# Performance work log

Measured on AMD Instinct MI355X. Metric: run time of the kernel, lower is better.

## Reference

```python
import jax, jax.numpy as jnp
import numpy as np

N_USERS, N_ITEMS, N_TOPICS = 200000, 100000, 100
N_NODES = N_USERS + N_ITEMS + N_TOPICS
N_EDGES = 5000000
DIM = 64
LAYERS = 3
BATCH = 16384


def setup_inputs() -> dict:
    key = jax.random.key(0)
    ks = jax.random.split(key, 8)
    users = jax.random.randint(ks[0], (BATCH,), 0, N_USERS, dtype=jnp.int64 if jax.config.jax_enable_x64 else jnp.int32)
    items = jax.random.randint(ks[1], (BATCH,), 0, N_ITEMS, dtype=jnp.int64 if jax.config.jax_enable_x64 else jnp.int32)
    edge_rows = jax.random.randint(ks[2], (N_EDGES,), 0, N_NODES, dtype=jnp.int32)
    edge_cols = jax.random.randint(ks[3], (N_EDGES,), 0, N_NODES, dtype=jnp.int32)
    # values ~ 1/deg to mimic the symmetric-normalized A_hat of LightGCN
    edge_vals = jax.random.uniform(ks[4], (N_EDGES,), dtype=jnp.float32) / 16.0
    user_emb = 0.1 * jax.random.normal(ks[5], (N_USERS, DIM), dtype=jnp.float32)
    item_emb = 0.1 * jax.random.normal(ks[6], (N_ITEMS, DIM), dtype=jnp.float32)
    topic_emb = 0.1 * jax.random.normal(ks[7], (N_TOPICS, DIM), dtype=jnp.float32)
    return {"users": users, "items": items, "edge_rows": edge_rows,
            "edge_cols": edge_cols, "edge_vals": edge_vals,
            "user_emb": user_emb, "item_emb": item_emb, "topic_emb": topic_emb}


def reference(users, items, edge_rows, edge_cols, edge_vals, user_emb, item_emb, topic_emb):
    n_users = user_emb.shape[0]
    n_nodes = n_users + item_emb.shape[0] + topic_emb.shape[0]
    # E^0 = [users; items; topics]
    h = jnp.concatenate([user_emb, item_emb, topic_emb], axis=0)  # [N, dim]
    acc = h
    for _ in range(LAYERS):
        # sparse A_hat @ h : gather source rows, scale by edge weight, scatter-add to dst
        msgs = edge_vals[:, None] * h[edge_cols]                  # [E, dim]
        h = jax.ops.segment_sum(msgs, edge_rows, num_segments=n_nodes)
        acc = acc + h
    out = acc / (LAYERS + 1)                                      # stack-mean over layers
    u = out[users]                                                # [B, dim]
    it = out[n_users + items]                                     # items offset into node table
    return jnp.sum(u * it, axis=1)                                # [B]
```

## Files before the change

kernel.cpp:

```cpp
#include <hip/hip_runtime.h>
#include <hip/hip_fp16.h>

#define N_USERS  200000
#define N_ITEMS  100000
#define N_TOPICS 100
#define N_NODES  (N_USERS + N_ITEMS + N_TOPICS)
#define DIM      64
#define BSHIFT   10
#define BROWS    (1 << BSHIFT)
#define NBUCKETS ((N_NODES + BROWS - 1) >> BSHIFT)
#define COLMASK  0x7FFFF
#define NB       512
#define NBSHIFT  9
#define M_TOT    (NBUCKETS * NB)
#define SB       256
#define CH       ((M_TOT + SB - 1) / SB)
#define BUCKET_CAP 24576



__global__ void prep_kernel(const int* __restrict__ rows,
                            int* __restrict__ partial, int n_edges,
                            const float* __restrict__ uemb,
                            const float* __restrict__ iemb,
                            const float* __restrict__ temb,
                            ushort* __restrict__ h0) {
    __shared__ int h[NBUCKETS];
    if (blockIdx.x < NB) {
        for (int i = threadIdx.x; i < NBUCKETS; i += blockDim.x) h[i] = 0;
        __syncthreads();
        int stride = NB * blockDim.x;
        for (int e = blockIdx.x * blockDim.x + threadIdx.x; e < n_edges; e += stride)
            atomicAdd(&h[((unsigned)rows[e]) >> BSHIFT], 1);
        __syncthreads();
        for (int i = threadIdx.x; i < NBUCKETS; i += blockDim.x)
            partial[blockIdx.x * NBUCKETS + i] = h[i];
    } else {
        int g = (blockIdx.x - NB) * blockDim.x + threadIdx.x;
        long base = (long)g * 4;
        if (base >= (long)N_NODES * DIM) return;
        const float* src;
        long off;
        if (base < (long)N_USERS * DIM)                 { src = uemb; off = base; }
        else if (base < (long)(N_USERS + N_ITEMS) * DIM){ src = iemb; off = base - (long)N_USERS * DIM; }
        else                                            { src = temb; off = base - (long)(N_USERS + N_ITEMS) * DIM; }
        float4 v = *(const float4*)(src + off);
        __half2 a = __floats2half2_rn(v.x, v.y);
        __half2 b = __floats2half2_rn(v.z, v.w);
        uint2 o;
        o.x = *(unsigned*)&a;
        o.y = *(unsigned*)&b;
        ((uint2*)h0)[g] = o;
    }
}

__device__ __forceinline__ int phys_idx(int L) {
    return (L & (NB - 1)) * NBUCKETS + (L >> NBSHIFT);
}

__global__ void scanB1_kernel(const int* __restrict__ partial,
                              int* __restrict__ psum) {
    __shared__ int s[256];
    int tid = threadIdx.x;
    int c0 = blockIdx.x * CH;
    int c1 = min(M_TOT, c0 + CH);
    int sum = 0;
    for (int L = c0 + tid; L < c1; L += 256) sum += partial[phys_idx(L)];
    s[tid] = sum;
    __syncthreads();
    for (int off = 128; off > 0; off >>= 1) {
        if (tid < off) s[tid] += s[tid + off];
        __syncthreads();
    }
    if (tid == 0) psum[blockIdx.x] = s[0];
}

__global__ void scanB3_kernel(const int* __restrict__ partial,
                              const int* __restrict__ psum,
                              int* __restrict__ offs) {
    __shared__ int s[SB];
    __shared__ int tile[256];
    __shared__ int carry;
    int tid = threadIdx.x;
    s[tid] = (tid < blockIdx.x) ? psum[tid] : 0;
    __syncthreads();
    for (int off = 128; off > 0; off >>= 1) {
        if (tid < off) s[tid] += s[tid + off];
        __syncthreads();
    }
    if (tid == 0) carry = s[0];
    __syncthreads();
    int c0 = blockIdx.x * CH;
    int c1 = min(M_TOT, c0 + CH);
    for (int base = c0; base < c1; base += 256) {
        int L = base + tid;
        int v = (L < c1) ? partial[phys_idx(L)] : 0;
        tile[tid] = v;
        __syncthreads();
        for (int off = 1; off < 256; off <<= 1) {
            int t = (tid >= off) ? tile[tid - off] : 0;
            __syncthreads();
            tile[tid] += t;
            __syncthreads();
        }
        if (L < c1) offs[L] = carry + tile[tid] - v;
        __syncthreads();
        if (tid == 255) carry += tile[255];
        __syncthreads();
    }
}

__global__ void scatter1_kernel(const int* __restrict__ rows,
                                const int* __restrict__ cols,
                                const float* __restrict__ vals,
                                const int* __restrict__ offs,
                                int2* __restrict__ bkt_buf, int n_edges) {
    __shared__ int lpos[NBUCKETS];
    for (int i = threadIdx.x; i < NBUCKETS; i += blockDim.x)
        lpos[i] = offs[i * NB + blockIdx.x];
    __syncthreads();
    int stride = gridDim.x * blockDim.x;
    for (int e = blockIdx.x * blockDim.x + threadIdx.x; e < n_edges; e += stride) {
        int r = rows[e];
        int b = ((unsigned)r) >> BSHIFT;
        int pos = atomicAdd(&lpos[b], 1);
        int2 p;
        p.x = cols[e] | ((r & (BROWS - 1)) << 19);
        p.y = __float_as_int(vals[e]);
        bkt_buf[pos] = p;
    }
}

__device__ __forceinline__ int pad8(int x) { return (x + 7) & ~7; }

__global__ void scatter2_kernel(const int2* __restrict__ bkt_buf,
                                const int* __restrict__ offs,
                                int2* __restrict__ row_span,
                                int2* __restrict__ csr_cv, int n_edges) {
    __shared__ int lcnt[BROWS];
    __shared__ int lptr[BROWS];
    __shared__ int lfill[BROWS];
    __shared__ int s[512];
    int b = blockIdx.x;
    int t = threadIdx.x;
    int e0 = offs[b * NB];
    int e1 = (b == NBUCKETS - 1) ? n_edges : offs[(b + 1) * NB];
    for (int i = t; i < BROWS; i += 512) { lcnt[i] = 0; lfill[i] = 0; }
    __syncthreads();
    for (int e = e0 + t; e < e1; e += blockDim.x)
        atomicAdd(&lcnt[((unsigned)bkt_buf[e].x) >> 19], 1);
    __syncthreads();
    s[t] = pad8(lcnt[2 * t]) + pad8(lcnt[2 * t + 1]);
    __syncthreads();
    for (int off = 1; off < 512; off <<= 1) {
        int v = (t >= off) ? s[t - off] : 0;
        __syncthreads();
        s[t] += v;
        __syncthreads();
    }
    {
        int base = b * BUCKET_CAP + (t ? s[t - 1] : 0);
        int rbase = b << BSHIFT;
        int pe = pad8(lcnt[2 * t]);
        int po = pad8(lcnt[2 * t + 1]);
        int p_even = base;
        int p_odd  = base + pe;
        lptr[2 * t]     = p_even;
        lptr[2 * t + 1] = p_odd;
        if (rbase + 2 * t < N_NODES) {
            int2 sp; sp.x = p_even; sp.y = p_even + pe;
            row_span[rbase + 2 * t] = sp;
        }
        if (rbase + 2 * t + 1 < N_NODES) {
            int2 sp; sp.x = p_odd; sp.y = p_odd + po;
            row_span[rbase + 2 * t + 1] = sp;
        }
    }
    __syncthreads();
    for (int e = e0 + t; e < e1; e += blockDim.x) {
        int2 p = bkt_buf[e];
        int delta = ((unsigned)p.x) >> 19;
        int pos = lptr[delta] + atomicAdd(&lfill[delta], 1);
        int2 cv;
        cv.x = p.x & COLMASK;
        cv.y = p.y;
        csr_cv[pos] = cv;
    }
    __syncthreads();
    for (int i = t; i < BROWS; i += 512) {
        int c  = lcnt[i];
        int cp = pad8(c);
        int p  = lptr[i];
        int2 z; z.x = 0; z.y = 0;
        for (int k = c; k < cp; ++k) csr_cv[p + k] = z;
    }
}

__device__ __forceinline__ float4 fma_mix4(const ushort* __restrict__ h,
                                           int row, int l16, float w,
                                           float4 acc) {
    uint2 r = ((const uint2*)(h + (size_t)row * DIM))[l16];
    __half2 h01 = *(__half2*)&r.x;
    __half2 h23 = *(__half2*)&r.y;
    acc.x = __builtin_fmaf(__half2float(__low2half(h01)),  w, acc.x);
    acc.y = __builtin_fmaf(__half2float(__high2half(h01)), w, acc.y);
    acc.z = __builtin_fmaf(__half2float(__low2half(h23)),  w, acc.z);
    acc.w = __builtin_fmaf(__half2float(__high2half(h23)), w, acc.w);
    return acc;
}

__device__ __forceinline__ float4 batch8(const int2* __restrict__ csr_cv,
                                         const ushort* __restrict__ h_src,
                                         int p, int l16, float4 acc) {
    const int4* q = (const int4*)(csr_cv + p);
    int4 a = q[0], b = q[1], c = q[2], d = q[3];
    acc = fma_mix4(h_src, a.x, l16, __int_as_float(a.y), acc);
    acc = fma_mix4(h_src, a.z, l16, __int_as_float(a.w), acc);
    acc = fma_mix4(h_src, b.x, l16, __int_as_float(b.y), acc);
    acc = fma_mix4(h_src, b.z, l16, __int_as_float(b.w), acc);
    acc = fma_mix4(h_src, c.x, l16, __int_as_float(c.y), acc);
    acc = fma_mix4(h_src, c.z, l16, __int_as_float(c.w), acc);
    acc = fma_mix4(h_src, d.x, l16, __int_as_float(d.y), acc);
    acc = fma_mix4(h_src, d.z, l16, __int_as_float(d.w), acc);
    return acc;
}

#define NWAVES ((N_NODES + 3) / 4)

__global__ void spmv_csr_kernel(const int2* __restrict__ row_span,
                                const int2* __restrict__ csr_cv,
                                const ushort* __restrict__ h_src,
                                ushort* __restrict__ h_dst,
                                const int* __restrict__ users,
                                const int* __restrict__ items,
                                float* __restrict__ u_acc,
                                float* __restrict__ it_acc,
                                int B, int first) {
    int wave = (int)(((long)blockIdx.x * blockDim.x + threadIdx.x) >> 6);
    int lane = threadIdx.x & 63;
    int g    = lane >> 4;
    int l16  = lane & 15;
    if (wave < NWAVES) {
        int r    = wave * 4 + g;
        int rc   = min(r, N_NODES - 1);
        int2 sp  = row_span[rc];
        int p0   = sp.x;
        int len  = (r < N_NODES) ? (sp.y - sp.x) : 0;
        int m = max(len, __shfl_xor(len, 16, 64));
        m = max(m, __shfl_xor(m, 32, 64));
        float4 acc = make_float4(0.f, 0.f, 0.f, 0.f);
        for (int off = 0; off < m; off += 8) {
            if (off < len)
                acc = batch8(csr_cv, h_src, p0 + off, l16, acc);
        }
        if (r < N_NODES) {
            __half2 a = __floats2half2_rn(acc.x, acc.y);
            __half2 b = __floats2half2_rn(acc.z, acc.w);
            uint2 o;
            o.x = *(unsigned*)&a;
            o.y = *(unsigned*)&b;
            ((uint2*)(h_dst + (size_t)r * DIM))[l16] = o;
        }
    } else {
        int s = (wave - NWAVES) * 4 + g;
        if (s >= 2 * B) return;
        int node = (s < B) ? users[s] : (N_USERS + items[s - B]);
        uint2 hr = ((const uint2*)(h_src + (size_t)node * DIM))[l16];
        float2 a01 = __half22float2(*(__half2*)&hr.x);
        float2 a23 = __half22float2(*(__half2*)&hr.y);
        float* dst = (s < B) ? (u_acc + (size_t)s * DIM)
                             : (it_acc + (size_t)(s - B) * DIM);
        float4* p = (float4*)dst + l16;
        if (first) {
            *p = make_float4(a01.x, a01.y, a23.x, a23.y);
        } else {
            float4 o = *p;
            o.x += a01.x; o.y += a01.y; o.z += a23.x; o.w += a23.y;
            *p = o;
        }
    }
}

__global__ void spmv_batch_kernel(const int2* __restrict__ row_span,
                                  const int2* __restrict__ csr_cv,
                                  const ushort* __restrict__ h_src,
                                  const int* __restrict__ users,
                                  const int* __restrict__ items,
                                  float* __restrict__ u_acc,
                                  float* __restrict__ it_acc, int B) {
    int wave = (int)(((long)blockIdx.x * blockDim.x + threadIdx.x) >> 6);
    int lane = threadIdx.x & 63;
    int g    = lane >> 4;
    int l16  = lane & 15;
    int s    = wave * 4 + g;
    bool ok  = s < 2 * B;
    int node = 0;
    if (ok) node = (s < B) ? users[s] : (N_USERS + items[s - B]);
    float4 acc = make_float4(0.f, 0.f, 0.f, 0.f);
    if (ok) {
        uint2 hr = ((const uint2*)(h_src + (size_t)node * DIM))[l16];
        float2 a01 = __half22float2(*(__half2*)&hr.x);
        float2 a23 = __half22float2(*(__half2*)&hr.y);
        acc = make_float4(a01.x, a01.y, a23.x, a23.y);
    }
    int2 sp  = row_span[node];
    int p0   = sp.x;
    int len  = ok ? (sp.y - sp.x) : 0;
    int m = max(len, __shfl_xor(len, 16, 64));
    m = max(m, __shfl_xor(m, 32, 64));
    for (int off = 0; off < m; off += 8) {
        if (off < len)
            acc = batch8(csr_cv, h_src, p0 + off, l16, acc);
    }
    if (ok) {
        float* dst = (s < B) ? (u_acc + (size_t)s * DIM)
                             : (it_acc + (size_t)(s - B) * DIM);
        float4* p = (float4*)dst + l16;
        float4 old = *p;
        old.x += acc.x; old.y += acc.y; old.z += acc.z; old.w += acc.w;
        *p = old;
    }
}

__global__ void dot_kernel(const float* __restrict__ u_acc,
                           const float* __restrict__ it_acc,
                           float* __restrict__ out, int B) {
    int gid  = blockIdx.x * blockDim.x + threadIdx.x;
    int b    = gid >> 6;
    int lane = gid & 63;
    if (b >= B) return;
    float p = u_acc[(size_t)b * DIM + lane] * it_acc[(size_t)b * DIM + lane];
    #pragma unroll
    for (int off = 32; off > 0; off >>= 1)
        p += __shfl_down(p, off, 64);
    if (lane == 0) out[b] = p * (1.0f / 16.0f);
}

extern "C" void kernel_launch(void* const* d_in, const int* in_sizes, int n_in,
                              void* d_out, int out_size, void* d_ws, size_t ws_size,
                              hipStream_t stream) {
    const int*   users = (const int*)d_in[0];
    const int*   items = (const int*)d_in[1];
    const int*   erows = (const int*)d_in[2];
    const int*   ecols = (const int*)d_in[3];
    const float* evals = (const float*)d_in[4];
    const float* uemb  = (const float*)d_in[5];
    const float* iemb  = (const float*)d_in[6];
    const float* temb  = (const float*)d_in[7];
    float* out = (float*)d_out;

    const int n_edges = in_sizes[2];
    const int B       = in_sizes[0];

    const size_t h2bytes = (((size_t)N_NODES * DIM * 2 + 255) / 256) * 256;
    const size_t abytes  = (size_t)B * DIM * sizeof(float);
    const size_t spbytes = (((size_t)N_NODES * 8 + 255) / 256) * 256;
    const size_t csrbytes= (size_t)NBUCKETS * BUCKET_CAP * 8;
    const size_t bkbytes = (size_t)n_edges * 8;
    const size_t mbytes  = (((size_t)M_TOT * 4 + 255) / 256) * 256;

    char* ws = (char*)d_ws;
    size_t off = 0;
    ushort* hA       = (ushort*)(ws + off); off += h2bytes;
    ushort* hB       = (ushort*)(ws + off); off += h2bytes;
    float*  u_acc    = (float*) (ws + off); off += abytes;
    float*  it_acc   = (float*) (ws + off); off += abytes;
    int2*   row_span = (int2*)  (ws + off); off += spbytes;
    int2*   csr_cv   = (int2*)  (ws + off); off += csrbytes;
    int2*   bkt_buf  = (int2*)  (ws + off); off += bkbytes;
    int*    partial  = (int*)   (ws + off); off += mbytes;
    int*    offs     = (int*)   (ws + off); off += mbytes;
    int*    psum     = (int*)   (ws + off); off += 4096;

    dim3 blk(256);
    dim3 blk512(512);

    const long n4 = (long)N_NODES * DIM / 4;
    const int  nconcat = (int)((n4 + 511) / 512);
    prep_kernel<<<NB + nconcat, blk512, 0, stream>>>(erows, partial, n_edges,
                                                     uemb, iemb, temb, hA);
    scanB1_kernel<<<SB, blk, 0, stream>>>(partial, psum);
    scanB3_kernel<<<SB, blk, 0, stream>>>(partial, psum, offs);
    scatter1_kernel<<<NB, blk512, 0, stream>>>(erows, ecols, evals, offs, bkt_buf, n_edges);
    scatter2_kernel<<<NBUCKETS, blk512, 0, stream>>>(bkt_buf, offs, row_span, csr_cv, n_edges);

    const int gwaves  = (2 * B + 3) / 4;
    const int fblocks = (int)(((long)(NWAVES + gwaves) * 64 + 255) / 256);
    spmv_csr_kernel<<<fblocks, blk, 0, stream>>>(row_span, csr_cv, hA, hB,
                                                 users, items, u_acc, it_acc, B, 1);
    spmv_csr_kernel<<<fblocks, blk, 0, stream>>>(row_span, csr_cv, hB, hA,
                                                 users, items, u_acc, it_acc, B, 0);
    const int bblocks = (int)(((long)gwaves * 64 + 255) / 256);
    spmv_batch_kernel<<<bblocks, blk, 0, stream>>>(row_span, csr_cv, hA,
                                                   users, items, u_acc, it_acc, B);

    dot_kernel<<<(B * 64 + 255) / 256, blk, 0, stream>>>(u_acc, it_acc, out, B);
}
```

Measured before the change: 524.4 us.

## Precompute per-row counts globally and split CSR scatter across more blocks

Per-row edge counts are now gathered with global atomics inside the existing histogram pass. A new scan kernel builds row spans, cursor arrays and zero padding from those counts. The second scatter pass drops its per-bucket shared-memory count, scan and fill phases and uses 8 blocks per bucket with global atomics on per-row cursors, which raises parallelism in that pass. The cost is millions of global atomics in prep and scatter2, plus an extra memset and kernel launch.

```diff
diff --git a/kernel.cpp b/kernel.cpp
--- a/kernel.cpp
+++ b/kernel.cpp
@@ -9,18 +9,21 @@
 #define BSHIFT   10
 #define BROWS    (1 << BSHIFT)
 #define NBUCKETS ((N_NODES + BROWS - 1) >> BSHIFT)
+#define NROWS_PAD (NBUCKETS * BROWS)
 #define COLMASK  0x7FFFF
 #define NB       512
 #define NBSHIFT  9
 #define M_TOT    (NBUCKETS * NB)
 #define SB       256
 #define CH       ((M_TOT + SB - 1) / SB)
+#define S2SPLIT  8
 #define BUCKET_CAP 24576
 
 
 
 __global__ void prep_kernel(const int* __restrict__ rows,
-                            int* __restrict__ partial, int n_edges,
+                            int* __restrict__ partial,
+                            int* __restrict__ row_cnt, int n_edges,
                             const float* __restrict__ uemb,
                             const float* __restrict__ iemb,
                             const float* __restrict__ temb,
@@ -30,8 +33,11 @@
         for (int i = threadIdx.x; i < NBUCKETS; i += blockDim.x) h[i] = 0;
         __syncthreads();
         int stride = NB * blockDim.x;
-        for (int e = blockIdx.x * blockDim.x + threadIdx.x; e < n_edges; e += stride)
-            atomicAdd(&h[((unsigned)rows[e]) >> BSHIFT], 1);
+        for (int e = blockIdx.x * blockDim.x + threadIdx.x; e < n_edges; e += stride) {
+            int r = rows[e];
+            atomicAdd(&h[((unsigned)r) >> BSHIFT], 1);
+            atomicAdd(&row_cnt[r], 1);
+        }
         __syncthreads();
         for (int i = threadIdx.x; i < NBUCKETS; i += blockDim.x)
             partial[blockIdx.x * NBUCKETS + i] = h[i];
@@ -110,6 +116,46 @@
     }
 }
 
+__device__ __forceinline__ int pad8(int x) { return (x + 7) & ~7; }
+
+__global__ void scanR_kernel(const int* __restrict__ row_cnt,
+                             int2* __restrict__ row_span,
+                             int* __restrict__ row_next,
+                             int2* __restrict__ csr_cv) {
+    __shared__ int lcnt[BROWS];
+    __shared__ int s[512];
+    int b = blockIdx.x;
+    int t = threadIdx.x;
+    int rbase = b << BSHIFT;
+    lcnt[t]       = row_cnt[rbase + t];
+    lcnt[t + 512] = row_cnt[rbase + t + 512];
+    __syncthreads();
+    s[t] = pad8(lcnt[2 * t]) + pad8(lcnt[2 * t + 1]);
+    __syncthreads();
+    for (int off = 1; off < 512; off <<= 1) {
+        int v = (t >= off) ? s[t - off] : 0;
+        __syncthreads();
+        s[t] += v;
+        __syncthreads();
+    }
+    int base = b * BUCKET_CAP + (t ? s[t - 1] : 0);
+    int c0 = lcnt[2 * t];
+    int c1 = lcnt[2 * t + 1];
+    int pe = pad8(c0);
+    int po = pad8(c1);
+    int p_even = base;
+    int p_odd  = base + pe;
+    int2 sp0; sp0.x = p_even; sp0.y = p_even + pe;
+    int2 sp1; sp1.x = p_odd;  sp1.y = p_odd + po;
+    row_span[rbase + 2 * t]     = sp0;
+    row_span[rbase + 2 * t + 1] = sp1;
+    row_next[rbase + 2 * t]     = p_even;
+    row_next[rbase + 2 * t + 1] = p_odd;
+    int2 z; z.x = 0; z.y = 0;
+    for (int k = c0; k < pe; ++k) csr_cv[p_even + k] = z;
+    for (int k = c1; k < po; ++k) csr_cv[p_odd + k]  = z;
+}
+
 __global__ void scatter1_kernel(const int* __restrict__ rows,
                                 const int* __restrict__ cols,
                                 const float* __restrict__ vals,
@@ -131,68 +177,24 @@
     }
 }
 
-__device__ __forceinline__ int pad8(int x) { return (x + 7) & ~7; }
-
 __global__ void scatter2_kernel(const int2* __restrict__ bkt_buf,
                                 const int* __restrict__ offs,
-                                int2* __restrict__ row_span,
+                                int* __restrict__ row_next,
                                 int2* __restrict__ csr_cv, int n_edges) {
-    __shared__ int lcnt[BROWS];
-    __shared__ int lptr[BROWS];
-    __shared__ int lfill[BROWS];
-    __shared__ int s[512];
-    int b = blockIdx.x;
-    int t = threadIdx.x;
+    int b = blockIdx.x / S2SPLIT;
+    int c = blockIdx.x % S2SPLIT;
     int e0 = offs[b * NB];
     int e1 = (b == NBUCKETS - 1) ? n_edges : offs[(b + 1) * NB];
-    for (int i = t; i < BROWS; i += 512) { lcnt[i] = 0; lfill[i] = 0; }
-    __syncthreads();
-    for (int e = e0 + t; e < e1; e += blockDim.x)
-        atomicAdd(&lcnt[((unsigned)bkt_buf[e].x) >> 19], 1);
-    __syncthreads();
-    s[t] = pad8(lcnt[2 * t]) + pad8(lcnt[2 * t + 1]);
-    __syncthreads();
-    for (int off = 1; off < 512; off <<= 1) {
-        int v = (t >= off) ? s[t - off] : 0;
-        __syncthreads();
-        s[t] += v;
-        __syncthreads();
-    }
-    {
-        int base = b * BUCKET_CAP + (t ? s[t - 1] : 0);
-        int rbase = b << BSHIFT;
-        int pe = pad8(lcnt[2 * t]);
-        int po = pad8(lcnt[2 * t + 1]);
-        int p_even = base;
-        int p_odd  = base + pe;
-        lptr[2 * t]     = p_even;
-        lptr[2 * t + 1] = p_odd;
-        if (rbase + 2 * t < N_NODES) {
-            int2 sp; sp.x = p_even; sp.y = p_even + pe;
-            row_span[rbase + 2 * t] = sp;
-        }
-        if (rbase + 2 * t + 1 < N_NODES) {
-            int2 sp; sp.x = p_odd; sp.y = p_odd + po;
-            row_span[rbase + 2 * t + 1] = sp;
-        }
-    }
-    __syncthreads();
-    for (int e = e0 + t; e < e1; e += blockDim.x) {
+    int rbase = b << BSHIFT;
+    for (int e = e0 + c * blockDim.x + threadIdx.x; e < e1;
+         e += S2SPLIT * blockDim.x) {
         int2 p = bkt_buf[e];
-        int delta = ((unsigned)p.x) >> 19;
-        int pos = lptr[delta] + atomicAdd(&lfill[delta], 1);
+        int row = rbase + (((unsigned)p.x) >> 19);
+        int pos = atomicAdd(&row_next[row], 1);
         int2 cv;
         cv.x = p.x & COLMASK;
         cv.y = p.y;
         csr_cv[pos] = cv;
-    }
-    __syncthreads();
-    for (int i = t; i < BROWS; i += 512) {
-        int c  = lcnt[i];
-        int cp = pad8(c);
-        int p  = lptr[i];
-        int2 z; z.x = 0; z.y = 0;
-        for (int k = c; k < cp; ++k) csr_cv[p + k] = z;
     }
 }
 
@@ -354,10 +356,11 @@
 
     const size_t h2bytes = (((size_t)N_NODES * DIM * 2 + 255) / 256) * 256;
     const size_t abytes  = (size_t)B * DIM * sizeof(float);
-    const size_t spbytes = (((size_t)N_NODES * 8 + 255) / 256) * 256;
+    const size_t spbytes = (((size_t)NROWS_PAD * 8 + 255) / 256) * 256;
     const size_t csrbytes= (size_t)NBUCKETS * BUCKET_CAP * 8;
     const size_t bkbytes = (size_t)n_edges * 8;
     const size_t mbytes  = (((size_t)M_TOT * 4 + 255) / 256) * 256;
+    const size_t cbytes  = (((size_t)NROWS_PAD * 4 + 255) / 256) * 256;
 
     char* ws = (char*)d_ws;
     size_t off = 0;
@@ -370,19 +373,24 @@
     int2*   bkt_buf  = (int2*)  (ws + off); off += bkbytes;
     int*    partial  = (int*)   (ws + off); off += mbytes;
     int*    offs     = (int*)   (ws + off); off += mbytes;
+    int*    row_cnt  = (int*)   (ws + off); off += cbytes;
+    int*    row_next = (int*)   (ws + off); off += cbytes;
     int*    psum     = (int*)   (ws + off); off += 4096;
 
     dim3 blk(256);
     dim3 blk512(512);
 
+    hipMemsetAsync(row_cnt, 0, (size_t)NROWS_PAD * 4, stream);
     const long n4 = (long)N_NODES * DIM / 4;
     const int  nconcat = (int)((n4 + 511) / 512);
-    prep_kernel<<<NB + nconcat, blk512, 0, stream>>>(erows, partial, n_edges,
-                                                     uemb, iemb, temb, hA);
+    prep_kernel<<<NB + nconcat, blk512, 0, stream>>>(erows, partial, row_cnt,
+                                                     n_edges, uemb, iemb, temb, hA);
     scanB1_kernel<<<SB, blk, 0, stream>>>(partial, psum);
     scanB3_kernel<<<SB, blk, 0, stream>>>(partial, psum, offs);
+    scanR_kernel<<<NBUCKETS, blk512, 0, stream>>>(row_cnt, row_span, row_next, csr_cv);
     scatter1_kernel<<<NB, blk512, 0, stream>>>(erows, ecols, evals, offs, bkt_buf, n_edges);
-    scatter2_kernel<<<NBUCKETS, blk512, 0, stream>>>(bkt_buf, offs, row_span, csr_cv, n_edges);
+    scatter2_kernel<<<NBUCKETS * S2SPLIT, blk, 0, stream>>>(bkt_buf, offs,
+                                                            row_next, csr_cv, n_edges);
 
     const int gwaves  = (2 * B + 3) / 4;
     const int fblocks = (int)(((long)(NWAVES + gwaves) * 64 + 255) / 256);
```

New measurement: 891.8 us. 70.1% more time.
